# Kernel tuning notes

Measured on AMD Instinct MI355X. Metric: run time of the kernel, lower is better.

The kernel has to match this reference:

```python
import jax, jax.numpy as jnp
import numpy as np

B, H, W, C, NC = 4, 64, 64, 64, 19


def setup_inputs() -> dict:
    key = jax.random.key(0)
    ks = jax.random.split(key, 12)
    s = 0.05  # small init so sigmoid scores are not saturated
    return {
        "feature": jax.random.normal(ks[0], (B, H, W, C), dtype=jnp.float32),
        "predict": jax.random.normal(ks[1], (B, H, W, NC), dtype=jnp.float32),
        # height attention params (dim = H); k_linear in source is unused (q reused as k)
        "hq_w": jax.random.normal(ks[2], (H, H), dtype=jnp.float32) * s,
        "hq_b": jnp.zeros((H,), dtype=jnp.float32),
        "hv_w": jax.random.normal(ks[3], (H, H), dtype=jnp.float32) * s,
        "hv_b": jnp.zeros((H,), dtype=jnp.float32),
        # width attention params (dim = W)
        "wq_w": jax.random.normal(ks[4], (W, W), dtype=jnp.float32) * s,
        "wq_b": jnp.zeros((W,), dtype=jnp.float32),
        "wv_w": jax.random.normal(ks[5], (W, W), dtype=jnp.float32) * s,
        "wv_b": jnp.zeros((W,), dtype=jnp.float32),
        # gating scalars (nn.Parameter(torch.zeros(1)) in source; random here to exercise path)
        "h_gate": jax.random.normal(ks[6], (1,), dtype=jnp.float32) * 0.5,
        "w_gate": jax.random.normal(ks[7], (1,), dtype=jnp.float32) * 0.5,
        # 1x1 conv num_classes -> 1 (stored as [NC, 1] matrix; 1x1 conv == per-pixel linear)
        "conv_w": jax.random.normal(ks[8], (NC, 1), dtype=jnp.float32) * s,
        "conv_b": jnp.zeros((1,), dtype=jnp.float32),
    }


def _self_atten(x, wq, bq, wv, bv, dim):
    # Source uses q_linear for BOTH q and k (k_linear dead), softmax replaced by sigmoid.
    q = x @ wq + bq                                   # [B, N, dim]
    v = x @ wv + bv                                   # [B, N, dim]
    scores = jax.nn.sigmoid(jnp.einsum('bnd,bmd->bnm', q, q) / jnp.sqrt(jnp.float32(dim)))
    return jnp.einsum('bnm,bmd->bnd', scores, v)      # [B, N, dim]


def _axial(x, hq_w, hq_b, hv_w, hv_b, wq_w, wq_b, wv_w, wv_b, h_gate, w_gate):
    b, h, w, c = x.shape
    # height attention: seq = W*C, feature dim = H
    xh = x.transpose(0, 2, 3, 1).reshape(b, w * c, h)
    xh = _self_atten(xh, hq_w, hq_b, hv_w, hv_b, h)
    xh = xh.reshape(b, w, c, h).transpose(0, 3, 1, 2)  # back to [B,H,W,C]
    x = xh * h_gate + x
    # width attention: seq = H*C, feature dim = W
    xw = x.transpose(0, 1, 3, 2).reshape(b, h * c, w)
    xw = _self_atten(xw, wq_w, wq_b, wv_w, wv_b, w)
    xw = xw.reshape(b, h, c, w).transpose(0, 1, 3, 2)  # back to [B,H,W,C]
    x = xw * w_gate + x
    return x


def reference(feature, predict, hq_w, hq_b, hv_w, hv_b, wq_w, wq_b, wv_w, wv_b,
              h_gate, w_gate, conv_w, conv_b):
    feat = feature + _axial(feature, hq_w, hq_b, hv_w, hv_b,
                            wq_w, wq_b, wv_w, wv_b, h_gate, w_gate)
    p = 1.0 - jax.nn.sigmoid(predict)                 # [B,H,W,NC]
    p = p @ conv_w + conv_b                           # 1x1 conv -> [B,H,W,1]
    return p * feat                                   # broadcast gate -> [B,H,W,C]
```

## Files before the change

### kernel.cpp

```cpp
#include <hip/hip_runtime.h>

typedef _Float16 f16x8 __attribute__((ext_vector_type(8)));
typedef __fp16   fp16x2 __attribute__((ext_vector_type(2)));
typedef float f32x16 __attribute__((ext_vector_type(16)));

__device__ __forceinline__ unsigned pkrtz(float a, float b) {
    fp16x2 h = __builtin_amdgcn_cvt_pkrtz(a, b);
    union { fp16x2 h; unsigned u; } c; c.h = h; return c.u;
}

__device__ __forceinline__ unsigned short f2h(float f) {
    _Float16 h = (_Float16)f;
    union { _Float16 h; unsigned short s; } c; c.h = h; return c.s;
}

__global__ __launch_bounds__(256) void prep_kernel(
    const float* __restrict__ src,
    const float* __restrict__ wq, const float* __restrict__ bq,
    const float* __restrict__ wv, const float* __restrict__ bv,
    unsigned short* __restrict__ Qg, unsigned short* __restrict__ Vtg)
{
    __shared__ float slab[64][65];
    __shared__ float wqs[4096];
    __shared__ float wvs[4096];

    const int t  = threadIdx.x;
    const int bx = blockIdx.x, b = blockIdx.y;

    {
        const float4* wq4 = (const float4*)wq;
        const float4* wv4 = (const float4*)wv;
        float4* q4 = (float4*)wqs; float4* v4 = (float4*)wvs;
        #pragma unroll
        for (int i = 0; i < 4; ++i) {
            q4[i*256 + t] = wq4[i*256 + t];
            v4[i*256 + t] = wv4[i*256 + t];
        }
    }
    {
        const int k = t >> 2, c0 = (t & 3) << 4;
        const size_t sb = (size_t)b*262144 + (size_t)k*4096 + (size_t)bx*64 + c0;
        #pragma unroll
        for (int i = 0; i < 4; ++i)
            *(float4*)&slab[k][c0 + i*4] = *(const float4*)&src[sb + i*4];
    }
    __syncthreads();

    const int c = t & 63, jg = t >> 6;
    float qa[16], va[16];
    #pragma unroll
    for (int jj = 0; jj < 16; ++jj) { qa[jj] = bq[jg*16+jj]; va[jj] = bv[jg*16+jj]; }
    for (int k = 0; k < 64; ++k) {
        const float xv = slab[k][c];
        const float* wqr = &wqs[k*64 + jg*16];
        const float* wvr = &wvs[k*64 + jg*16];
        #pragma unroll
        for (int jj = 0; jj < 16; ++jj) {
            qa[jj] += xv * wqr[jj];
            va[jj] += xv * wvr[jj];
        }
    }
    const int token = bx*64 + c;
    union { unsigned u[8]; uint4 v[2]; } qp;
    #pragma unroll
    for (int jj = 0; jj < 8; ++jj) qp.u[jj] = pkrtz(qa[2*jj], qa[2*jj+1]);
    const size_t qoff = ((size_t)b*4096 + token)*64 + jg*16;
    *(uint4*)&Qg[qoff]     = qp.v[0];
    *(uint4*)&Qg[qoff + 8] = qp.v[1];
    #pragma unroll
    for (int jj = 0; jj < 16; ++jj)
        Vtg[((size_t)b*64 + jg*16 + jj)*4096 + token] = f2h(va[jj]);
}

__global__ __launch_bounds__(256) void prep_w_kernel(
    const float* __restrict__ feature, const float* __restrict__ Pin,
    const float* __restrict__ gate,
    const float* __restrict__ wq, const float* __restrict__ bq,
    const float* __restrict__ wv, const float* __restrict__ bv,
    unsigned short* __restrict__ Qg, unsigned short* __restrict__ Vtg,
    float* __restrict__ x1out, int nsplit)
{
    __shared__ float slab[64][65];
    __shared__ float wqs[4096];
    __shared__ float wvs[4096];

    const int t  = threadIdx.x;
    const int bx = blockIdx.x, b = blockIdx.y;

    {
        const float4* wq4 = (const float4*)wq;
        const float4* wv4 = (const float4*)wv;
        float4* q4 = (float4*)wqs; float4* v4 = (float4*)wvs;
        #pragma unroll
        for (int i = 0; i < 4; ++i) {
            q4[i*256 + t] = wq4[i*256 + t];
            v4[i*256 + t] = wv4[i*256 + t];
        }
    }
    {
        const int k = t >> 2, c0 = (t & 3) << 4;
        const size_t off = (size_t)bx*4096 + (size_t)k*64 + c0;
        const size_t fb  = (size_t)b*262144 + off;
        const float g = gate[0];
        #pragma unroll
        for (int i = 0; i < 4; ++i) {
            float4 v  = *(const float4*)&feature[fb + i*4];
            float sx = 0.f, sy = 0.f, sz = 0.f, sw = 0.f;
            for (int ks = 0; ks < nsplit; ++ks) {
                float4 pk = *(const float4*)&Pin[((size_t)(ks*4 + b) << 18) + off + i*4];
                sx += pk.x; sy += pk.y; sz += pk.z; sw += pk.w;
            }
            v.x += g * sx; v.y += g * sy; v.z += g * sz; v.w += g * sw;
            *(float4*)&slab[k][c0 + i*4] = v;
            *(float4*)&x1out[fb + i*4] = v;
        }
    }
    __syncthreads();

    const int c = t & 63, jg = t >> 6;
    float qa[16], va[16];
    #pragma unroll
    for (int jj = 0; jj < 16; ++jj) { qa[jj] = bq[jg*16+jj]; va[jj] = bv[jg*16+jj]; }
    for (int k = 0; k < 64; ++k) {
        const float xv = slab[k][c];
        const float* wqr = &wqs[k*64 + jg*16];
        const float* wvr = &wvs[k*64 + jg*16];
        #pragma unroll
        for (int jj = 0; jj < 16; ++jj) {
            qa[jj] += xv * wqr[jj];
            va[jj] += xv * wvr[jj];
        }
    }
    const int token = bx*64 + c;
    union { unsigned u[8]; uint4 v[2]; } qp;
    #pragma unroll
    for (int jj = 0; jj < 8; ++jj) qp.u[jj] = pkrtz(qa[2*jj], qa[2*jj+1]);
    const size_t qoff = ((size_t)b*4096 + token)*64 + jg*16;
    *(uint4*)&Qg[qoff]     = qp.v[0];
    *(uint4*)&Qg[qoff + 8] = qp.v[1];
    #pragma unroll
    for (int jj = 0; jj < 16; ++jj)
        Vtg[((size_t)b*64 + jg*16 + jj)*4096 + token] = f2h(va[jj]);
}

__global__ __launch_bounds__(256) void attn_kernel(
    const unsigned short* __restrict__ Qg,
    const unsigned short* __restrict__ Vtg,
    float* __restrict__ P)
{
    __shared__ unsigned short Ksh[2][64][72];
    __shared__ unsigned short Vts[2][64][72];

    const int t = threadIdx.x;
    const int mb = blockIdx.x, b = blockIdx.y, ksplit = blockIdx.z;
    const int nsp = gridDim.z;
    const int niter = 64 / nsp;
    const int keybase = ksplit * (4096 / nsp);
    const int lane = t & 63, w = t >> 6;
    const int l32 = lane & 31, hi = lane >> 5;

    const unsigned short* Qbase = Qg  + (size_t)b*262144;
    const unsigned short* Vbase = Vtg + (size_t)b*262144;

    f16x8 qb[4];
    {
        const unsigned short* qrow = Qbase + (size_t)(mb*128 + w*32 + l32)*64 + hi*8;
        const _Float16 sc = (_Float16)(-0.180336880f);
        #pragma unroll
        for (int s = 0; s < 4; ++s) {
            f16x8 q = *(const f16x8*)(qrow + s*16);
            qb[s] = q * sc;
        }
    }

    f32x16 y[2];
    #pragma unroll
    for (int i = 0; i < 16; ++i) { y[0][i] = 0.f; y[1][i] = 0.f; }

    const int lrow = t >> 2;
    const int loff = (t & 3) << 4;
    {
        const uint4* gk = (const uint4*)(Qbase + (size_t)(keybase + lrow)*64 + loff);
        uint4 k0 = gk[0], k1 = gk[1];
        const uint4* gv = (const uint4*)(Vbase + (size_t)lrow*4096 + keybase + loff);
        uint4 v0 = gv[0], v1 = gv[1];
        *(uint4*)&Ksh[0][lrow][loff]     = k0;
        *(uint4*)&Ksh[0][lrow][loff + 8] = k1;
        uint4 pa = { v0.x, v0.y, v1.x, v1.y };
        uint4 pb = { v0.z, v0.w, v1.z, v1.w };
        *(uint4*)&Vts[0][lrow][loff]     = pa;
        *(uint4*)&Vts[0][lrow][loff + 8] = pb;
    }
    __syncthreads();

    for (int kb = 0; kb < niter; ++kb) {
        const int cur = kb & 1, nxt = cur ^ 1;

        uint4 nk0 = {0,0,0,0}, nk1 = {0,0,0,0}, nv0 = {0,0,0,0}, nv1 = {0,0,0,0};
        if (kb < niter - 1) {
            const int keyn = keybase + (kb + 1)*64;
            const uint4* gk = (const uint4*)(Qbase + (size_t)(keyn + lrow)*64 + loff);
            nk0 = gk[0]; nk1 = gk[1];
            const uint4* gv = (const uint4*)(Vbase + (size_t)lrow*4096 + keyn + loff);
            nv0 = gv[0]; nv1 = gv[1];
        }

        f32x16 tt[2];
        #pragma unroll
        for (int i = 0; i < 16; ++i) { tt[0][i] = 0.f; tt[1][i] = 0.f; }
        #pragma unroll
        for (int s = 0; s < 4; ++s) {
            const int co = s*16 + hi*8;
            f16x8 ka0 = *(const f16x8*)&Ksh[cur][l32][co];
            f16x8 ka1 = *(const f16x8*)&Ksh[cur][32 + l32][co];
            tt[0] = __builtin_amdgcn_mfma_f32_32x32x16_f16(ka0, qb[s], tt[0], 0,0,0);
            tt[1] = __builtin_amdgcn_mfma_f32_32x32x16_f16(ka1, qb[s], tt[1], 0,0,0);
        }

        #pragma unroll
        for (int u = 0; u < 2; ++u) {
            unsigned pk_[8];
            #pragma unroll
            for (int pr = 0; pr < 8; ++pr) {
                float t0 = __builtin_fminf(tt[u][2*pr+0], 60.0f);
                float t1 = __builtin_fminf(tt[u][2*pr+1], 60.0f);
                float e0 = __builtin_exp2f(t0);
                float e1 = __builtin_exp2f(t1);
                float d0 = 1.0f + e0, d1 = 1.0f + e1;
                float rr = __builtin_amdgcn_rcpf(d0 * d1);
                pk_[pr] = pkrtz(rr * d1, rr * d0);
            }
            #pragma unroll
            for (int sp = 0; sp < 2; ++sp) {
                union { unsigned u4[4]; f16x8 v; } sa;
                sa.u4[0] = pk_[sp*4 + 0];
                sa.u4[1] = pk_[sp*4 + 1];
                sa.u4[2] = pk_[sp*4 + 2];
                sa.u4[3] = pk_[sp*4 + 3];
                const int ks = u*2 + sp;
                const int co = ks*16 + hi*8;
                f16x8 vb0 = *(const f16x8*)&Vts[cur][l32][co];
                f16x8 vb1 = *(const f16x8*)&Vts[cur][32 + l32][co];
                y[0] = __builtin_amdgcn_mfma_f32_32x32x16_f16(sa.v, vb0, y[0], 0,0,0);
                y[1] = __builtin_amdgcn_mfma_f32_32x32x16_f16(sa.v, vb1, y[1], 0,0,0);
            }
        }

        if (kb < niter - 1) {
            *(uint4*)&Ksh[nxt][lrow][loff]     = nk0;
            *(uint4*)&Ksh[nxt][lrow][loff + 8] = nk1;
            uint4 pa = { nv0.x, nv0.y, nv1.x, nv1.y };
            uint4 pb = { nv0.z, nv0.w, nv1.z, nv1.w };
            *(uint4*)&Vts[nxt][lrow][loff]     = pa;
            *(uint4*)&Vts[nxt][lrow][loff + 8] = pb;
        }
        __syncthreads();
    }

    float* Pp = P + (((size_t)(ksplit*4 + b)) << 18);
    const int token0 = mb*128 + w*32 + hi*4;
    #pragma unroll
    for (int dt = 0; dt < 2; ++dt) {
        const int d = dt*32 + l32;
        #pragma unroll
        for (int g = 0; g < 4; ++g) {
            float4 v;
            v.x = y[dt][4*g+0]; v.y = y[dt][4*g+1];
            v.z = y[dt][4*g+2]; v.w = y[dt][4*g+3];
            *(float4*)&Pp[(size_t)d*4096 + token0 + 8*g] = v;
        }
    }
}

__global__ __launch_bounds__(256) void final_kernel(
    const float* __restrict__ feature, const float* __restrict__ x1,
    const float* __restrict__ Pin, const float* __restrict__ predict,
    const float* __restrict__ conv_w, const float* __restrict__ conv_b,
    const float* __restrict__ gate, float* __restrict__ out, int nsplit)
{
    const int i4 = blockIdx.x * 256 + threadIdx.x;
    const int j = i4 << 2;
    const int pix = j >> 6;
    const float* row = predict + (size_t)pix * 19;
    float pv = conv_b[0];
    #pragma unroll
    for (int i = 0; i < 19; ++i) {
        float sg = __builtin_amdgcn_rcpf(1.0f + __builtin_exp2f(-1.442695041f * row[i]));
        pv += (1.0f - sg) * conv_w[i];
    }

    const int b = j >> 18, h = (j >> 12) & 63, d = (j >> 6) & 63, c = j & 63;
    const size_t pif = ((size_t)(b*64 + d) << 12) + h*64 + c;
    float sx = 0.f, sy = 0.f, sz = 0.f, sw = 0.f;
    for (int ks = 0; ks < nsplit; ++ks) {
        float4 pk = *(const float4*)&Pin[((size_t)ks << 20) + pif];
        sx += pk.x; sy += pk.y; sz += pk.z; sw += pk.w;
    }
    const float g = gate[0];
    float4 f = ((const float4*)feature)[i4];
    float4 x = ((const float4*)x1)[i4];
    float4 o;
    o.x = pv * (f.x + x.x + g * sx);
    o.y = pv * (f.y + x.y + g * sy);
    o.z = pv * (f.z + x.z + g * sz);
    o.w = pv * (f.w + x.w + g * sw);
    ((float4*)out)[i4] = o;
}

extern "C" void kernel_launch(void* const* d_in, const int* in_sizes, int n_in,
                              void* d_out, int out_size, void* d_ws, size_t ws_size,
                              hipStream_t stream) {
    const float* feature = (const float*)d_in[0];
    const float* predict = (const float*)d_in[1];
    const float* hq_w = (const float*)d_in[2];
    const float* hq_b = (const float*)d_in[3];
    const float* hv_w = (const float*)d_in[4];
    const float* hv_b = (const float*)d_in[5];
    const float* wq_w = (const float*)d_in[6];
    const float* wq_b = (const float*)d_in[7];
    const float* wv_w = (const float*)d_in[8];
    const float* wv_b = (const float*)d_in[9];
    const float* h_gate = (const float*)d_in[10];
    const float* w_gate = (const float*)d_in[11];
    const float* conv_w = (const float*)d_in[12];
    const float* conv_b = (const float*)d_in[13];
    float* out = (float*)d_out;

    char* ws = (char*)d_ws;
    unsigned short* Qg  = (unsigned short*)(ws);
    unsigned short* Vtg = (unsigned short*)(ws + (2u << 20));
    float*          x1  = (float*)(ws + (4u << 20));
    float*          P   = (float*)(ws + (8u << 20));
    const int nsplit = 4;

    dim3 blk(256);
    prep_kernel<<<dim3(64, 4), blk, 0, stream>>>(feature, hq_w, hq_b, hv_w, hv_b,
                                                 Qg, Vtg);
    attn_kernel<<<dim3(32, 4, nsplit), blk, 0, stream>>>(Qg, Vtg, P);
    prep_w_kernel<<<dim3(64, 4), blk, 0, stream>>>(feature, P, h_gate,
                                                   wq_w, wq_b, wv_w, wv_b,
                                                   Qg, Vtg, x1, nsplit);
    attn_kernel<<<dim3(32, 4, nsplit), blk, 0, stream>>>(Qg, Vtg, P);
    final_kernel<<<dim3(1024), blk, 0, stream>>>(feature, x1, P, predict,
                                                 conv_w, conv_b, w_gate, out, nsplit);
}
```

Baseline: 189.4 us.

## Single-buffer LDS tiles in attention kernel, add MFMA priority and zero-init accumulator

Replaces the double-buffered K/V shared-memory tiles with single buffers, halving LDS use per block so more blocks can be resident per CU. Register prefetch from global memory still overlaps compute, but the LDS store now needs two barriers per iteration instead of one. The compute phase is wrapped in s_setprio to favour MFMA issue. The first QK MFMA takes a zero accumulator directly rather than clearing tt by hand. The trade-off is extra synchronisation in exchange for higher occupancy.

```diff
diff --git a/kernel.cpp b/kernel.cpp
--- a/kernel.cpp
+++ b/kernel.cpp
@@ -148,8 +148,8 @@
     const unsigned short* __restrict__ Vtg,
     float* __restrict__ P)
 {
-    __shared__ unsigned short Ksh[2][64][72];
-    __shared__ unsigned short Vts[2][64][72];
+    __shared__ unsigned short Ksh[64][72];
+    __shared__ unsigned short Vts[64][72];
 
     const int t = threadIdx.x;
     const int mb = blockIdx.x, b = blockIdx.y, ksplit = blockIdx.z;
@@ -173,9 +173,12 @@
         }
     }
 
+    f32x16 fz;
+    #pragma unroll
+    for (int i = 0; i < 16; ++i) fz[i] = 0.f;
+
     f32x16 y[2];
-    #pragma unroll
-    for (int i = 0; i < 16; ++i) { y[0][i] = 0.f; y[1][i] = 0.f; }
+    y[0] = fz; y[1] = fz;
 
     const int lrow = t >> 2;
     const int loff = (t & 3) << 4;
@@ -184,18 +187,16 @@
         uint4 k0 = gk[0], k1 = gk[1];
         const uint4* gv = (const uint4*)(Vbase + (size_t)lrow*4096 + keybase + loff);
         uint4 v0 = gv[0], v1 = gv[1];
-        *(uint4*)&Ksh[0][lrow][loff]     = k0;
-        *(uint4*)&Ksh[0][lrow][loff + 8] = k1;
+        *(uint4*)&Ksh[lrow][loff]     = k0;
+        *(uint4*)&Ksh[lrow][loff + 8] = k1;
         uint4 pa = { v0.x, v0.y, v1.x, v1.y };
         uint4 pb = { v0.z, v0.w, v1.z, v1.w };
-        *(uint4*)&Vts[0][lrow][loff]     = pa;
-        *(uint4*)&Vts[0][lrow][loff + 8] = pb;
+        *(uint4*)&Vts[lrow][loff]     = pa;
+        *(uint4*)&Vts[lrow][loff + 8] = pb;
     }
     __syncthreads();
 
     for (int kb = 0; kb < niter; ++kb) {
-        const int cur = kb & 1, nxt = cur ^ 1;
-
         uint4 nk0 = {0,0,0,0}, nk1 = {0,0,0,0}, nv0 = {0,0,0,0}, nv1 = {0,0,0,0};
         if (kb < niter - 1) {
             const int keyn = keybase + (kb + 1)*64;
@@ -205,16 +206,21 @@
             nv0 = gv[0]; nv1 = gv[1];
         }
 
+        __builtin_amdgcn_s_setprio(1);
+
         f32x16 tt[2];
-        #pragma unroll
-        for (int i = 0; i < 16; ++i) { tt[0][i] = 0.f; tt[1][i] = 0.f; }
         #pragma unroll
         for (int s = 0; s < 4; ++s) {
             const int co = s*16 + hi*8;
-            f16x8 ka0 = *(const f16x8*)&Ksh[cur][l32][co];
-            f16x8 ka1 = *(const f16x8*)&Ksh[cur][32 + l32][co];
-            tt[0] = __builtin_amdgcn_mfma_f32_32x32x16_f16(ka0, qb[s], tt[0], 0,0,0);
-            tt[1] = __builtin_amdgcn_mfma_f32_32x32x16_f16(ka1, qb[s], tt[1], 0,0,0);
+            f16x8 ka0 = *(const f16x8*)&Ksh[l32][co];
+            f16x8 ka1 = *(const f16x8*)&Ksh[32 + l32][co];
+            if (s == 0) {
+                tt[0] = __builtin_amdgcn_mfma_f32_32x32x16_f16(ka0, qb[0], fz, 0,0,0);
+                tt[1] = __builtin_amdgcn_mfma_f32_32x32x16_f16(ka1, qb[0], fz, 0,0,0);
+            } else {
+                tt[0] = __builtin_amdgcn_mfma_f32_32x32x16_f16(ka0, qb[s], tt[0], 0,0,0);
+                tt[1] = __builtin_amdgcn_mfma_f32_32x32x16_f16(ka1, qb[s], tt[1], 0,0,0);
+            }
         }
 
         #pragma unroll
@@ -239,22 +245,25 @@
                 sa.u4[3] = pk_[sp*4 + 3];
                 const int ks = u*2 + sp;
                 const int co = ks*16 + hi*8;
-                f16x8 vb0 = *(const f16x8*)&Vts[cur][l32][co];
-                f16x8 vb1 = *(const f16x8*)&Vts[cur][32 + l32][co];
+                f16x8 vb0 = *(const f16x8*)&Vts[l32][co];
+                f16x8 vb1 = *(const f16x8*)&Vts[32 + l32][co];
                 y[0] = __builtin_amdgcn_mfma_f32_32x32x16_f16(sa.v, vb0, y[0], 0,0,0);
                 y[1] = __builtin_amdgcn_mfma_f32_32x32x16_f16(sa.v, vb1, y[1], 0,0,0);
             }
         }
 
+        __builtin_amdgcn_s_setprio(0);
+
         if (kb < niter - 1) {
-            *(uint4*)&Ksh[nxt][lrow][loff]     = nk0;
-            *(uint4*)&Ksh[nxt][lrow][loff + 8] = nk1;
+            __syncthreads();
+            *(uint4*)&Ksh[lrow][loff]     = nk0;
+            *(uint4*)&Ksh[lrow][loff + 8] = nk1;
             uint4 pa = { nv0.x, nv0.y, nv1.x, nv1.y };
             uint4 pb = { nv0.z, nv0.w, nv1.z, nv1.w };
-            *(uint4*)&Vts[nxt][lrow][loff]     = pa;
-            *(uint4*)&Vts[nxt][lrow][loff + 8] = pb;
-        }
-        __syncthreads();
+            *(uint4*)&Vts[lrow][loff]     = pa;
+            *(uint4*)&Vts[lrow][loff + 8] = pb;
+            __syncthreads();
+        }
     }
 
     float* Pp = P + (((size_t)(ksplit*4 + b)) << 18);
```

After: 190.9 us. No clear change (+0.8%).

## Replace transcendental exp2/rcp with VALU polynomial and Newton approximations in sigmoid

Applied to the files above, without the earlier changes.

Replaces the hardware exp2 and rcp instructions in the attention sigmoid and the final-kernel sigmoid with a degree-4 polynomial exp2 plus ldexp and a bit-trick reciprocal refined by two Newton steps. This moves the work off the quarter-rate transcendental unit onto full-rate FMA units. The change also feeds the first MFMA a zero accumulator instead of zero-initialising tt every iteration, raises wave priority around the compute section, and lowers the exponent clamp from 60 to 30. The approximations add many VALU instructions and carry some accuracy risk.

```diff
diff --git a/kernel.cpp b/kernel.cpp
--- a/kernel.cpp
+++ b/kernel.cpp
@@ -12,6 +12,26 @@
 __device__ __forceinline__ unsigned short f2h(float f) {
     _Float16 h = (_Float16)f;
     union { _Float16 h; unsigned short s; } c; c.h = h; return c.s;
+}
+
+__device__ __forceinline__ float exp2v(float t) {
+    float fl = __builtin_floorf(t);
+    float f  = t - fl;
+    int   n  = (int)fl;
+    float p  = __builtin_fmaf(f, 0.0111222f, 0.05550411f);
+    p = __builtin_fmaf(p, f, 0.24022651f);
+    p = __builtin_fmaf(p, f, 0.69314718f);
+    p = __builtin_fmaf(p, f, 1.0f);
+    return __builtin_ldexpf(p, n);
+}
+
+__device__ __forceinline__ float rcpv(float d) {
+    union { float f; unsigned u; } c; c.f = d;
+    c.u = 0x7EF311C3u - c.u;
+    float r = c.f;
+    r = r * __builtin_fmaf(-d, r, 2.0f);
+    r = r * __builtin_fmaf(-d, r, 2.0f);
+    return r;
 }
 
 __global__ __launch_bounds__(256) void prep_kernel(
@@ -173,9 +193,12 @@
         }
     }
 
+    f32x16 fz;
+    #pragma unroll
+    for (int i = 0; i < 16; ++i) fz[i] = 0.f;
+
     f32x16 y[2];
-    #pragma unroll
-    for (int i = 0; i < 16; ++i) { y[0][i] = 0.f; y[1][i] = 0.f; }
+    y[0] = fz; y[1] = fz;
 
     const int lrow = t >> 2;
     const int loff = (t & 3) << 4;
@@ -205,16 +228,21 @@
             nv0 = gv[0]; nv1 = gv[1];
         }
 
+        __builtin_amdgcn_s_setprio(1);
+
         f32x16 tt[2];
-        #pragma unroll
-        for (int i = 0; i < 16; ++i) { tt[0][i] = 0.f; tt[1][i] = 0.f; }
         #pragma unroll
         for (int s = 0; s < 4; ++s) {
             const int co = s*16 + hi*8;
             f16x8 ka0 = *(const f16x8*)&Ksh[cur][l32][co];
             f16x8 ka1 = *(const f16x8*)&Ksh[cur][32 + l32][co];
-            tt[0] = __builtin_amdgcn_mfma_f32_32x32x16_f16(ka0, qb[s], tt[0], 0,0,0);
-            tt[1] = __builtin_amdgcn_mfma_f32_32x32x16_f16(ka1, qb[s], tt[1], 0,0,0);
+            if (s == 0) {
+                tt[0] = __builtin_amdgcn_mfma_f32_32x32x16_f16(ka0, qb[0], fz, 0,0,0);
+                tt[1] = __builtin_amdgcn_mfma_f32_32x32x16_f16(ka1, qb[0], fz, 0,0,0);
+            } else {
+                tt[0] = __builtin_amdgcn_mfma_f32_32x32x16_f16(ka0, qb[s], tt[0], 0,0,0);
+                tt[1] = __builtin_amdgcn_mfma_f32_32x32x16_f16(ka1, qb[s], tt[1], 0,0,0);
+            }
         }
 
         #pragma unroll
@@ -222,12 +250,12 @@
             unsigned pk_[8];
             #pragma unroll
             for (int pr = 0; pr < 8; ++pr) {
-                float t0 = __builtin_fminf(tt[u][2*pr+0], 60.0f);
-                float t1 = __builtin_fminf(tt[u][2*pr+1], 60.0f);
-                float e0 = __builtin_exp2f(t0);
-                float e1 = __builtin_exp2f(t1);
+                float t0 = __builtin_fminf(tt[u][2*pr+0], 30.0f);
+                float t1 = __builtin_fminf(tt[u][2*pr+1], 30.0f);
+                float e0 = exp2v(t0);
+                float e1 = exp2v(t1);
                 float d0 = 1.0f + e0, d1 = 1.0f + e1;
-                float rr = __builtin_amdgcn_rcpf(d0 * d1);
+                float rr = rcpv(d0 * d1);
                 pk_[pr] = pkrtz(rr * d1, rr * d0);
             }
             #pragma unroll
@@ -246,6 +274,8 @@
             }
         }
 
+        __builtin_amdgcn_s_setprio(0);
+
         if (kb < niter - 1) {
             *(uint4*)&Ksh[nxt][lrow][loff]     = nk0;
             *(uint4*)&Ksh[nxt][lrow][loff + 8] = nk1;
@@ -285,8 +315,9 @@
     float pv = conv_b[0];
     #pragma unroll
     for (int i = 0; i < 19; ++i) {
-        float sg = __builtin_amdgcn_rcpf(1.0f + __builtin_exp2f(-1.442695041f * row[i]));
-        pv += (1.0f - sg) * conv_w[i];
+        float tt = __builtin_fminf(row[i] * 1.442695041f, 30.0f);
+        float q  = rcpv(1.0f + exp2v(tt));
+        pv = __builtin_fmaf(q, conv_w[i], pv);
     }
 
     const int b = j >> 18, h = (j >> 12) & 63, d = (j >> 6) & 63, c = j & 63;
```

After: 191.3 us. Within noise of the previous version (+1.0%).
